# Optimization experiments

Hardware: AMD Instinct MI355X
Metric: run time of the kernel (lower is better)

Reference implementation:

```python
import jax, jax.numpy as jnp
import numpy as np

N_LAYERS = 3
FEATS = 128
POS = 3
M_DIM = 64
E_IN = 1 + 2 * FEATS          # 257 (rel_dist + x_i + x_j)
N_NODES = 20000
N_EDGES = 320000
LN_EPS = 1e-5


def _xavier(key, shape):
    fan_in, fan_out = shape[0], shape[1]
    std = (2.0 / (fan_in + fan_out)) ** 0.5
    return jax.random.normal(key, shape, dtype=jnp.float32) * std


def setup_inputs() -> dict:
    key = jax.random.key(0)
    ks = jax.random.split(key, 10)
    x = jax.random.normal(ks[0], (N_NODES, POS + FEATS), dtype=jnp.float32)
    edge_index = jax.random.randint(ks[1], (2, N_EDGES), 0, N_NODES)
    L = N_LAYERS
    def stack(k, shape):
        return jax.vmap(lambda kk: _xavier(kk, shape))(jax.random.split(k, L))
    params = {
        "ew1": stack(ks[2], (E_IN, 2 * E_IN)),      # edge_mlp linear 1
        "eb1": jnp.zeros((L, 2 * E_IN), jnp.float32),
        "ew2": stack(ks[3], (2 * E_IN, M_DIM)),      # edge_mlp linear 2
        "eb2": jnp.zeros((L, M_DIM), jnp.float32),
        "ng": jnp.ones((L, FEATS), jnp.float32),     # node LayerNorm gamma
        "nb": jnp.zeros((L, FEATS), jnp.float32),    # node LayerNorm beta
        "nw1": stack(ks[4], (FEATS + M_DIM, 2 * FEATS)),
        "nb1": jnp.zeros((L, 2 * FEATS), jnp.float32),
        "nw2": stack(ks[5], (2 * FEATS, FEATS)),
        "nb2": jnp.zeros((L, FEATS), jnp.float32),
        "cw1": stack(ks[6], (M_DIM, 4 * M_DIM)),
        "cb1": jnp.zeros((L, 4 * M_DIM), jnp.float32),
        "cw2": stack(ks[7], (4 * M_DIM, 1)),
        "cb2": jnp.zeros((L, 1), jnp.float32),
    }
    return {"x": x, "edge_index": edge_index, **params}


def _layer(x, edge_index, ew1, eb1, ew2, eb2, ng, nb, nw1, nb1, nw2, nb2,
           cw1, cb1, cw2, cb2):
    coors, feats = x[:, :POS], x[:, POS:]
    src, dst = edge_index[0], edge_index[1]
    # relative geometry per edge
    rel_coors = coors[src] - coors[dst]                       # [E, 3]
    rel_dist = jnp.sum(rel_coors * rel_coors, axis=-1, keepdims=True)  # [E, 1]
    # message MLP: cat[x_i (target), x_j (source), rel_dist]
    e_in = jnp.concatenate([feats[dst], feats[src], rel_dist], axis=-1)
    h = jax.nn.silu(e_in @ ew1 + eb1)
    m_ij = jax.nn.silu(h @ ew2 + eb2)                         # [E, m_dim]
    # coordinate update
    coor_w = jax.nn.silu(m_ij @ cw1 + cb1) @ cw2 + cb2        # [E, 1]
    mhat = jax.ops.segment_sum(coor_w * rel_coors, dst, num_segments=N_NODES)
    coors_out = coors + mhat
    # feature update (LayerNorm then MLP, residual)
    m_i = jax.ops.segment_sum(m_ij, dst, num_segments=N_NODES)
    mu = jnp.mean(feats, axis=-1, keepdims=True)
    var = jnp.mean((feats - mu) ** 2, axis=-1, keepdims=True)
    feats_n = (feats - mu) * jax.lax.rsqrt(var + LN_EPS) * ng + nb
    n_in = jnp.concatenate([feats_n, m_i], axis=-1)
    nh = jax.nn.silu(n_in @ nw1 + nb1) @ nw2 + nb2
    feats_out = feats + nh
    return jnp.concatenate([coors_out, feats_out], axis=-1)


def reference(x, edge_index, ew1, eb1, ew2, eb2, ng, nb, nw1, nb1, nw2, nb2,
              cw1, cb1, cw2, cb2):
    for l in range(N_LAYERS):
        x = _layer(x, edge_index,
                   ew1[l], eb1[l], ew2[l], eb2[l],
                   ng[l], nb[l], nw1[l], nb1[l], nw2[l], nb2[l],
                   cw1[l], cb1[l], cw2[l], cb2[l])
    return x
```

## Files before the change

### kernel.cpp

```cpp
#include <hip/hip_runtime.h>

typedef unsigned short u16;
typedef unsigned int   u32;
typedef __attribute__((ext_vector_type(2))) u32  u32x2;
typedef __attribute__((ext_vector_type(4))) u32  u32x4;
typedef __attribute__((ext_vector_type(8))) __bf16 bf16x8;
typedef __attribute__((ext_vector_type(4))) float  f32x4;

#define NN 20000
#define NE 320000
#define XD 131
#define F  128
#define MD 64
#define H1 514
#define H1P 544
#define NCH 17

#define GAS __attribute__((address_space(1)))
#define LAS __attribute__((address_space(3)))
#define LGKM0 asm volatile("s_waitcnt lgkmcnt(0)" ::: "memory")
#define VM0   asm volatile("s_waitcnt vmcnt(0)" ::: "memory")

__device__ __forceinline__ float silu(float a) {
    float e = __expf(-a);
    return a * __builtin_amdgcn_rcpf(1.0f + e);
}

__device__ __forceinline__ u16 f2bf(float f) {
    u32 u = __builtin_bit_cast(u32, f);
    return (u16)((u + 0x7FFFu + ((u >> 16) & 1u)) >> 16);
}
__device__ __forceinline__ u16 bfc(float f) { return __builtin_bit_cast(u16, (__bf16)f); }
__device__ __forceinline__ u32 pk2(float a, float b) {
    return (u32)bfc(a) | ((u32)bfc(b) << 16);
}
__device__ __forceinline__ bf16x8 mk8(u32 a, u32 b, u32 c, u32 d) {
    u32x4 t = {a, b, c, d};
    return __builtin_bit_cast(bf16x8, t);
}
__device__ __forceinline__ f32x4 mfma16(bf16x8 a, bf16x8 b, f32x4 c) {
    return __builtin_amdgcn_mfma_f32_16x16x32_bf16(a, b, c, 0, 0, 0);
}


__global__ void prep_w1(const float* __restrict__ ew1, const float* __restrict__ eb1,
                        u16* __restrict__ w1b, float* __restrict__ bias2) {
    int i = blockIdx.x * 256 + threadIdx.x;
    if (i >= 3 * H1P * 256) return;
    int k = i & 255;
    int n = (i >> 8) % H1P;
    int l = (i >> 8) / H1P;
    float v = (n < H1) ? ew1[(size_t)l * 257 * H1 + (size_t)k * H1 + n] : 0.f;
    w1b[(size_t)(l * H1P + n) * 256 + (k ^ ((n & 7) << 3))] = f2bf(v);
    if (k == 0) {
        bias2[(l * H1P + n) * 2 + 0] = (n < H1) ? eb1[l * H1 + n] : 0.f;
        bias2[(l * H1P + n) * 2 + 1] = (n < H1) ? ew1[(size_t)l * 257 * H1 + (size_t)256 * H1 + n] : 0.f;
    }
}

__global__ void prep_w2(const float* __restrict__ ew2, u16* __restrict__ w2b) {
    int i = blockIdx.x * 256 + threadIdx.x;
    if (i >= 3 * 64 * H1P) return;
    int k = i % H1P;
    int n = (i / H1P) & 63;
    int l = i / (H1P * 64);
    float v = (k < H1) ? ew2[(size_t)l * H1 * 64 + (size_t)k * 64 + n] : 0.f;
    w2b[(size_t)(l * 64 + n) * H1P + k] = f2bf(v);
}

__global__ void prep_cw1(const float* __restrict__ cw1, u16* __restrict__ cw1b) {
    int i = blockIdx.x * 256 + threadIdx.x;
    if (i >= 3 * 256 * 64) return;
    int k = i & 63;
    int n = (i >> 6) & 255;
    int l = i >> 14;
    cw1b[(size_t)l * 16384 + n * 64 + k] = f2bf(cw1[(size_t)l * 16384 + k * 256 + n]);
}

__global__ void prep_nw1(const float* __restrict__ nw1, u16* __restrict__ nw1b) {
    int i = blockIdx.x * 256 + threadIdx.x;
    if (i >= 3 * 256 * 192) return;
    int k = i % 192;
    int n = (i / 192) & 255;
    int l = i / (192 * 256);
    nw1b[(size_t)(l * 256 + n) * 192 + k] = f2bf(nw1[(size_t)l * 192 * 256 + (size_t)k * 256 + n]);
}

__global__ void prep_nw2(const float* __restrict__ nw2, u16* __restrict__ nw2b) {
    int i = blockIdx.x * 256 + threadIdx.x;
    if (i >= 3 * 128 * 256) return;
    int k = i & 255;
    int n = (i >> 8) & 127;
    int l = i >> 15;
    nw2b[(size_t)(l * 128 + n) * 256 + k] = f2bf(nw2[(size_t)l * 256 * 128 + (size_t)k * 128 + n]);
}

__global__ void x2bf(const float* __restrict__ xc, u32* __restrict__ xbf) {
    int i = blockIdx.x * 256 + threadIdx.x;
    if (i >= NN * 64) return;
    const int node = i >> 6, p = i & 63;
    const float a = xc[(size_t)node * XD + 3 + 2 * p];
    const float b = xc[(size_t)node * XD + 4 + 2 * p];
    xbf[(size_t)node * 64 + p] = pk2(a, b);
}


__global__ void csr_hist(const int* __restrict__ eidx, int* __restrict__ cnt) {
    int e = blockIdx.x * 256 + threadIdx.x;
    if (e < NE) atomicAdd(&cnt[eidx[NE + e]], 1);
}

__global__ void csr_scan(const int* __restrict__ cnt, int* __restrict__ rowp) {
    __shared__ int ps[1024];
    const int t = threadIdx.x;
    const int base = t * 20;
    int loc[20];
    int s = 0;
    #pragma unroll
    for (int i = 0; i < 20; ++i) {
        const int idx = base + i;
        const int c = (idx < NN) ? cnt[idx] : 0;
        loc[i] = s;
        s += c;
    }
    ps[t] = s;
    __syncthreads();
    for (int off = 1; off < 1024; off <<= 1) {
        int v = (t >= off) ? ps[t - off] : 0;
        __syncthreads();
        ps[t] += v;
        __syncthreads();
    }
    const int segbase = (t > 0) ? ps[t - 1] : 0;
    #pragma unroll
    for (int i = 0; i < 20; ++i) {
        const int idx = base + i;
        if (idx < NN) rowp[idx] = segbase + loc[i];
    }
    if (t == 1023) rowp[NN] = ps[1023];
}

__global__ void csr_fill(const int* __restrict__ eidx, const int* __restrict__ rowp,
                         int* __restrict__ fill, int* __restrict__ eids) {
    int e = blockIdx.x * 256 + threadIdx.x;
    if (e >= NE) return;
    const int d = eidx[NE + e];
    const int pos = atomicAdd(&fill[d], 1);
    eids[rowp[d] + pos] = e;
}


__global__ __launch_bounds__(256, 4) void reduce_mi(
    const u16* __restrict__ gmij, const int* __restrict__ rowp,
    const int* __restrict__ eids, float* __restrict__ m_i) {
    const int tid = threadIdx.x;
    const int n = blockIdx.x * 4 + (tid >> 6);
    const int c = tid & 63;
    if (n >= NN) return;
    const int b = rowp[n], e = rowp[n + 1];
    float acc = 0.f;
    for (int j = b; j < e; ++j) {
        const int eid = eids[j];
        const u16 v = gmij[(size_t)eid * 64 + c];
        acc += __builtin_bit_cast(float, (u32)v << 16);
    }
    m_i[(size_t)n * 64 + c] = acc;
}


__global__ __launch_bounds__(256, 3) void edge_mfma(
    const float* __restrict__ x, const u16* __restrict__ xbf, const int* __restrict__ eidx,
    const char* __restrict__ w1b, const float* __restrict__ bias2,
    const char* __restrict__ w2b, const float* __restrict__ eb2,
    const char* __restrict__ cw1b, const float* __restrict__ cb1,
    const float* __restrict__ cw2, const float* __restrict__ cb2,
    float* __restrict__ m_i, float* __restrict__ mhat, u16* __restrict__ gmij)
{
    __shared__ __align__(16) char LDS[45568];
    const int tid = threadIdx.x;
    const int w = tid >> 6, l = tid & 63, lg = l >> 4, lc = l & 15;
    const int ebase = blockIdx.x * 128 + w * 32;
    char*  HT  = LDS + 32768 + w * 2560;
    char*  MJ  = LDS + w * 4352;
    float* RDS = (float*)(LDS + 43008);
    int*   SDS = (int*)(LDS + 45056);
    char*  STG = LDS + w * 8192;

    if (l < 32) {
        const int e = ebase + l;
        const int s = eidx[e], d = eidx[NE + e];
        const float ax = x[(size_t)s * XD + 0] - x[(size_t)d * XD + 0];
        const float ay = x[(size_t)s * XD + 1] - x[(size_t)d * XD + 1];
        const float az = x[(size_t)s * XD + 2] - x[(size_t)d * XD + 2];
        f32x4 v = {ax, ay, az, ax * ax + ay * ay + az * az};
        *(f32x4*)(RDS + (w * 32 + l) * 4) = v;
        SDS[w * 32 + l] = d;
    }

    bf16x8 A[2][8];
    const int r4 = l >> 4;
    #pragma unroll
    for (int p = 0; p < 2; ++p) {
        const int ebs = (p ? 0 : NE) + ebase;
        #pragma unroll
        for (int j = 0; j < 8; ++j) {
            const int r = j * 4 + r4;
            const int node = eidx[ebs + r];
            const int cp = lc ^ (r & 7);
            __builtin_amdgcn_global_load_lds((const GAS u32*)(xbf + (size_t)node * 128 + cp * 8),
                                             (LAS u32*)(STG + j * 1024), 16, 0, 0);
        }
        VM0;
        #pragma unroll
        for (int kt = 0; kt < 4; ++kt)
            #pragma unroll
            for (int et = 0; et < 2; ++et) {
                const int R = et * 16 + lc;
                A[et][p * 4 + kt] = *(bf16x8*)(STG + R * 256 + ((kt * 64 + lg * 16) ^ ((R & 7) << 4)));
            }
        LGKM0;
    }

    float rd_e[2];
    rd_e[0] = RDS[(w * 32 + lc) * 4 + 3];
    rd_e[1] = RDS[(w * 32 + 16 + lc) * 4 + 3];
    LGKM0;

    __syncthreads();

    f32x4 c2[2][4];
    #pragma unroll
    for (int nt = 0; nt < 4; ++nt) {
        const float b = eb2[nt * 16 + lc];
        c2[0][nt] = (f32x4){b, b, b, b};
        c2[1][nt] = (f32x4){b, b, b, b};
    }

    {
        const char* g = w1b + (size_t)w * 4096;
        #pragma unroll
        for (int r = 0; r < 4; ++r)
            __builtin_amdgcn_global_load_lds((const GAS u32*)(g + r * 1024 + l * 16),
                                             (LAS u32*)(LDS + w * 4096 + r * 1024), 16, 0, 0);
    }

    const float* pB = bias2;
    #pragma unroll 1
    for (int ch = 0; ch < NCH; ++ch) {
        VM0;
        __syncthreads();
        if (ch + 1 < NCH) {
            const char* g = w1b + (size_t)(ch + 1) * 16384 + w * 4096;
            char* dst = LDS + ((ch + 1) & 1) * 16384 + w * 4096;
            #pragma unroll
            for (int r = 0; r < 4; ++r)
                __builtin_amdgcn_global_load_lds((const GAS u32*)(g + r * 1024 + l * 16),
                                                 (LAS u32*)(dst + r * 1024), 16, 0, 0);
        }
        char* Bc = LDS + (ch & 1) * 16384;

        #pragma unroll
        for (int nt = 0; nt < 2; ++nt) {
            const float* bp = pB + (nt * 16 + lg * 4) * 2;
            f32x4 q0 = *(const f32x4*)(bp);
            f32x4 q1 = *(const f32x4*)(bp + 4);
            f32x4 c10, c11;
            c10[0] = fmaf(rd_e[0], q0[1], q0[0]); c10[1] = fmaf(rd_e[0], q0[3], q0[2]);
            c10[2] = fmaf(rd_e[0], q1[1], q1[0]); c10[3] = fmaf(rd_e[0], q1[3], q1[2]);
            c11[0] = fmaf(rd_e[1], q0[1], q0[0]); c11[1] = fmaf(rd_e[1], q0[3], q0[2]);
            c11[2] = fmaf(rd_e[1], q1[1], q1[0]); c11[3] = fmaf(rd_e[1], q1[3], q1[2]);
            const int nl = nt * 16 + lc;
            #pragma unroll
            for (int kt = 0; kt < 8; ++kt) {
                bf16x8 Wf = *(bf16x8*)(Bc + nl * 512 + ((kt * 64 + lg * 16) ^ ((nl & 7) << 4)));
                c10 = mfma16(Wf, A[0][kt], c10);
                c11 = mfma16(Wf, A[1][kt], c11);
            }
            u32x2 v0, v1;
            v0[0] = pk2(silu(c10[0]), silu(c10[1])); v0[1] = pk2(silu(c10[2]), silu(c10[3]));
            v1[0] = pk2(silu(c11[0]), silu(c11[1])); v1[1] = pk2(silu(c11[2]), silu(c11[3]));
            *(u32x2*)(HT + lc * 80 + nt * 32 + lg * 8) = v0;
            *(u32x2*)(HT + (16 + lc) * 80 + nt * 32 + lg * 8) = v1;
        }
        LGKM0;
        bf16x8 A2[2];
        A2[0] = *(bf16x8*)(HT + lc * 80 + lg * 16);
        A2[1] = *(bf16x8*)(HT + (16 + lc) * 80 + lg * 16);
        #pragma unroll
        for (int nt = 0; nt < 4; ++nt) {
            bf16x8 Bw = __builtin_bit_cast(bf16x8,
                *(const u32x4*)(w2b + (size_t)(nt * 16 + lc) * 1088 + ch * 64 + lg * 16));
            c2[0][nt] = mfma16(A2[0], Bw, c2[0][nt]);
            c2[1][nt] = mfma16(A2[1], Bw, c2[1][nt]);
        }
        pB += 64;
    }

    __syncthreads();

    int dstn[2][4];
    #pragma unroll
    for (int mt = 0; mt < 2; ++mt)
        #pragma unroll
        for (int r = 0; r < 4; ++r)
            dstn[mt][r] = SDS[w * 32 + mt * 16 + lg * 4 + r];

    #pragma unroll
    for (int mt = 0; mt < 2; ++mt)
        #pragma unroll
        for (int nt = 0; nt < 4; ++nt)
            #pragma unroll
            for (int r = 0; r < 4; ++r) {
                const float v = silu(c2[mt][nt][r]);
                const int rowl = mt * 16 + lg * 4 + r;
                const int col  = nt * 16 + lc;
                *(u16*)(MJ + rowl * 136 + col * 2) = bfc(v);
                if (!gmij) atomicAdd(m_i + (size_t)dstn[mt][r] * 64 + col, v);
            }
    LGKM0;

    if (gmij) {
        u16* grow = gmij + (size_t)ebase * 64;
        #pragma unroll
        for (int i = 0; i < 4; ++i) {
            const int row = i * 8 + (l >> 3);
            u32x4 v = *(u32x4*)(MJ + row * 136 + (l & 7) * 16);
            *(u32x4*)(grow + (size_t)row * 64 + (l & 7) * 8) = v;
        }
    }

    bf16x8 A3[2][2];
    #pragma unroll
    for (int mt = 0; mt < 2; ++mt)
        #pragma unroll
        for (int kt = 0; kt < 2; ++kt)
            A3[mt][kt] = *(bf16x8*)(MJ + (mt * 16 + lc) * 136 + kt * 64 + lg * 16);

    float pw[2][4] = {{0.f, 0.f, 0.f, 0.f}, {0.f, 0.f, 0.f, 0.f}};
    #pragma unroll 4
    for (int ct3 = 0; ct3 < 16; ++ct3) {
        const int col = ct3 * 16 + lc;
        const float b = cb1[col];
        f32x4 c30 = {b, b, b, b}, c31 = {b, b, b, b};
        #pragma unroll
        for (int kt = 0; kt < 2; ++kt) {
            bf16x8 B = __builtin_bit_cast(bf16x8,
                *(const u32x4*)(cw1b + (size_t)col * 128 + kt * 64 + lg * 16));
            c30 = mfma16(A3[0][kt], B, c30);
            c31 = mfma16(A3[1][kt], B, c31);
        }
        const float w2v = cw2[col];
        #pragma unroll
        for (int r = 0; r < 4; ++r) {
            pw[0][r] = fmaf(silu(c30[r]), w2v, pw[0][r]);
            pw[1][r] = fmaf(silu(c31[r]), w2v, pw[1][r]);
        }
    }
    #pragma unroll
    for (int m = 1; m < 16; m <<= 1)
        #pragma unroll
        for (int mt = 0; mt < 2; ++mt)
            #pragma unroll
            for (int r = 0; r < 4; ++r)
                pw[mt][r] += __shfl_xor(pw[mt][r], m, 64);

    const float cb2v = cb2[0];
    if (lc < 3) {
        #pragma unroll
        for (int mt = 0; mt < 2; ++mt)
            #pragma unroll
            for (int r = 0; r < 4; ++r) {
                const int rowl = mt * 16 + lg * 4 + r;
                const float cwv = pw[mt][r] + cb2v;
                atomicAdd(mhat + (size_t)dstn[mt][r] * 3 + lc,
                          cwv * RDS[(w * 32 + rowl) * 4 + lc]);
            }
    }
}


__global__ __launch_bounds__(256, 2) void node_mfma(
    const float* __restrict__ xc, const float* __restrict__ m_i, const float* __restrict__ mh,
    const float* __restrict__ ng, const float* __restrict__ nb,
    const char* __restrict__ nw1b, const float* __restrict__ nb1,
    const char* __restrict__ nw2b, const float* __restrict__ nb2,
    float* __restrict__ xn)
{
    __shared__ __align__(16) char LDS[4 * 4352];
    const int tid = threadIdx.x;
    const int w = tid >> 6, l = tid & 63, lg = l >> 4, lc = l & 15;
    char* HB = LDS + w * 4352;
    const int nb0 = blockIdx.x * 128 + w * 32;

    int nodes[2]; bool valid[2];
    #pragma unroll
    for (int et = 0; et < 2; ++et) {
        int n = nb0 + et * 16 + lc;
        valid[et] = (n < NN);
        nodes[et] = valid[et] ? n : (NN - 1);
    }

    bf16x8 BF[2][6];
    #pragma unroll
    for (int et = 0; et < 2; ++et) {
        const float* xr = xc + (size_t)nodes[et] * XD + 3;
        float v[4][8];
        float s = 0.f, q = 0.f;
        #pragma unroll
        for (int kt = 0; kt < 4; ++kt) {
            const int k0 = kt * 32 + lg * 8;
            #pragma unroll
            for (int j = 0; j < 8; ++j) {
                const float t = xr[k0 + j];
                v[kt][j] = t; s += t; q = fmaf(t, t, q);
            }
        }
        s += __shfl_xor(s, 16, 64); s += __shfl_xor(s, 32, 64);
        q += __shfl_xor(q, 16, 64); q += __shfl_xor(q, 32, 64);
        const float mu = s * (1.f / 128.f);
        const float rs = rsqrtf(q * (1.f / 128.f) - mu * mu + 1e-5f);
        #pragma unroll
        for (int kt = 0; kt < 4; ++kt) {
            const int k0 = kt * 32 + lg * 8;
            float4 g0 = *(const float4*)(ng + k0), g1 = *(const float4*)(ng + k0 + 4);
            float4 b0 = *(const float4*)(nb + k0), b1 = *(const float4*)(nb + k0 + 4);
            const u32 u0 = pk2((v[kt][0] - mu) * rs * g0.x + b0.x, (v[kt][1] - mu) * rs * g0.y + b0.y);
            const u32 u1 = pk2((v[kt][2] - mu) * rs * g0.z + b0.z, (v[kt][3] - mu) * rs * g0.w + b0.w);
            const u32 u2 = pk2((v[kt][4] - mu) * rs * g1.x + b1.x, (v[kt][5] - mu) * rs * g1.y + b1.y);
            const u32 u3 = pk2((v[kt][6] - mu) * rs * g1.z + b1.z, (v[kt][7] - mu) * rs * g1.w + b1.w);
            BF[et][kt] = mk8(u0, u1, u2, u3);
        }
        const float* mr = m_i + (size_t)nodes[et] * 64;
        #pragma unroll
        for (int kt2 = 0; kt2 < 2; ++kt2) {
            float4 a = *(const float4*)(mr + kt2 * 32 + lg * 8);
            float4 b = *(const float4*)(mr + kt2 * 32 + lg * 8 + 4);
            BF[et][4 + kt2] = mk8(pk2(a.x, a.y), pk2(a.z, a.w), pk2(b.x, b.y), pk2(b.z, b.w));
        }
    }

    f32x4 a2[8][2];
    #pragma unroll
    for (int ct2 = 0; ct2 < 8; ++ct2) {
        f32x4 b = *(const f32x4*)(nb2 + ct2 * 16 + lg * 4);
        a2[ct2][0] = b; a2[ct2][1] = b;
    }

    #pragma unroll 1
    for (int g = 0; g < 4; ++g) {
        f32x4 a1[4][2];
        #pragma unroll
        for (int ct = 0; ct < 4; ++ct) {
            f32x4 b = *(const f32x4*)(nb1 + g * 64 + ct * 16 + lg * 4);
            a1[ct][0] = b; a1[ct][1] = b;
        }
        #pragma unroll
        for (int ct = 0; ct < 4; ++ct)
            #pragma unroll
            for (int kt = 0; kt < 6; ++kt) {
                bf16x8 Aw = __builtin_bit_cast(bf16x8, *(const u32x4*)(
                    nw1b + (size_t)(g * 64 + ct * 16 + lc) * 384 + kt * 64 + lg * 16));
                a1[ct][0] = mfma16(Aw, BF[0][kt], a1[ct][0]);
                a1[ct][1] = mfma16(Aw, BF[1][kt], a1[ct][1]);
            }
        #pragma unroll
        for (int ct = 0; ct < 4; ++ct)
            #pragma unroll
            for (int et = 0; et < 2; ++et) {
                f32x4 c = a1[ct][et];
                u32 v0 = pk2(silu(c[0]), silu(c[1]));
                u32 v1 = pk2(silu(c[2]), silu(c[3]));
                *(u32*)(HB + (et * 16 + lc) * 136 + ct * 32 + lg * 8) = v0;
                *(u32*)(HB + (et * 16 + lc) * 136 + ct * 32 + lg * 8 + 4) = v1;
            }
        LGKM0;
        __builtin_amdgcn_sched_barrier(0);
        bf16x8 B2[2][2];
        #pragma unroll
        for (int et = 0; et < 2; ++et)
            #pragma unroll
            for (int kt2 = 0; kt2 < 2; ++kt2) {
                u32 a = *(u32*)(HB + (et * 16 + lc) * 136 + kt2 * 64 + lg * 16);
                u32 b = *(u32*)(HB + (et * 16 + lc) * 136 + kt2 * 64 + lg * 16 + 4);
                u32 c = *(u32*)(HB + (et * 16 + lc) * 136 + kt2 * 64 + lg * 16 + 8);
                u32 d = *(u32*)(HB + (et * 16 + lc) * 136 + kt2 * 64 + lg * 16 + 12);
                B2[et][kt2] = mk8(a, b, c, d);
            }
        #pragma unroll
        for (int ct2 = 0; ct2 < 8; ++ct2)
            #pragma unroll
            for (int kt2 = 0; kt2 < 2; ++kt2) {
                bf16x8 Aw = __builtin_bit_cast(bf16x8, *(const u32x4*)(
                    nw2b + (size_t)(ct2 * 16 + lc) * 512 + (g * 64 + kt2 * 32 + lg * 8) * 2));
                a2[ct2][0] = mfma16(Aw, B2[0][kt2], a2[ct2][0]);
                a2[ct2][1] = mfma16(Aw, B2[1][kt2], a2[ct2][1]);
            }
        LGKM0;
        __builtin_amdgcn_sched_barrier(0);
    }

    #pragma unroll
    for (int et = 0; et < 2; ++et) {
        if (!valid[et]) continue;
        const size_t nr = (size_t)nodes[et] * XD;
        #pragma unroll
        for (int ct2 = 0; ct2 < 8; ++ct2)
            #pragma unroll
            for (int r = 0; r < 4; ++r) {
                const int col = ct2 * 16 + lg * 4 + r;
                xn[nr + 3 + col] = a2[ct2][et][r] + xc[nr + 3 + col];
            }
    }
    for (int idx = tid; idx < 384; idx += 256) {
        const int n = blockIdx.x * 128 + idx / 3;
        const int d = idx - (idx / 3) * 3;
        if (n < NN)
            xn[(size_t)n * XD + d] = xc[(size_t)n * XD + d] + mh[n * 3 + d];
    }
}


extern "C" void kernel_launch(void* const* d_in, const int* in_sizes, int n_in,
                              void* d_out, int out_size, void* d_ws, size_t ws_size,
                              hipStream_t stream) {
    const float* x_in = (const float*)d_in[0];
    const int*   eidx = (const int*)  d_in[1];
    const float* ew1  = (const float*)d_in[2];
    const float* eb1  = (const float*)d_in[3];
    const float* ew2  = (const float*)d_in[4];
    const float* eb2  = (const float*)d_in[5];
    const float* ng   = (const float*)d_in[6];
    const float* nb   = (const float*)d_in[7];
    const float* nw1  = (const float*)d_in[8];
    const float* nb1  = (const float*)d_in[9];
    const float* nw2  = (const float*)d_in[10];
    const float* nb2  = (const float*)d_in[11];
    const float* cw1  = (const float*)d_in[12];
    const float* cb1  = (const float*)d_in[13];
    const float* cw2  = (const float*)d_in[14];
    const float* cb2  = (const float*)d_in[15];
    float* out = (float*)d_out;

    char* ws = (char*)d_ws;
    size_t off = 0;
    auto alloc = [&](size_t bytes) { char* p = ws + off; off = (off + bytes + 255) & ~255ull; return p; };
    float* mi    = (float*)alloc((size_t)NN * MD * 4);
    float* mh    = (float*)alloc((size_t)NN * 3 * 4);
    u32*   xbf   = (u32*)  alloc((size_t)NN * 256);
    float* bias2 = (float*)alloc((size_t)3 * H1P * 8);
    char*  w1b   = alloc((size_t)3 * H1P * 512);
    char*  w2b   = alloc((size_t)3 * 64 * 1088);
    char*  cw1b  = alloc((size_t)3 * 256 * 128);
    char*  nw1b  = alloc((size_t)3 * 256 * 384);
    char*  nw2b  = alloc((size_t)3 * 128 * 512);
    u16* gmij = (u16*)alloc((size_t)NE * 64 * 2);
    int* rowp = (int*) alloc((size_t)(NN + 1) * 4);
    int* eids = (int*) alloc((size_t)NE * 4);
    int* cnt  = (int*) alloc((size_t)NN * 4);
    int* fillp= (int*) alloc((size_t)NN * 4);
    const bool two = (off <= ws_size);

    prep_w1 <<<(3 * H1P * 256 + 255) / 256, 256, 0, stream>>>(ew1, eb1, (u16*)w1b, bias2);
    prep_w2 <<<(3 * 64 * H1P + 255) / 256, 256, 0, stream>>>(ew2, (u16*)w2b);
    prep_cw1<<<(3 * 256 * 64 + 255) / 256, 256, 0, stream>>>(cw1, (u16*)cw1b);
    prep_nw1<<<(3 * 256 * 192 + 255) / 256, 256, 0, stream>>>(nw1, (u16*)nw1b);
    prep_nw2<<<(3 * 128 * 256 + 255) / 256, 256, 0, stream>>>(nw2, (u16*)nw2b);

    if (two) {
        hipMemsetAsync(cnt,  0, (size_t)NN * 4, stream);
        hipMemsetAsync(fillp,0, (size_t)NN * 4, stream);
        csr_hist<<<(NE + 255) / 256, 256, 0, stream>>>(eidx, cnt);
        csr_scan<<<1, 1024, 0, stream>>>(cnt, rowp);
        csr_fill<<<(NE + 255) / 256, 256, 0, stream>>>(eidx, rowp, fillp, eids);
    }

    for (int l = 0; l < 3; ++l) {
        const float* xc = (l == 0) ? x_in : out;
        float*       xn = out;
        if (!two) hipMemsetAsync(mi, 0, (size_t)NN * MD * 4, stream);
        hipMemsetAsync(mh, 0, (size_t)NN * 3 * 4, stream);
        x2bf<<<(NN * 64 + 255) / 256, 256, 0, stream>>>(xc, xbf);
        edge_mfma<<<NE / 128, 256, 0, stream>>>(
            xc, (const u16*)xbf, eidx,
            w1b + (size_t)l * H1P * 512, bias2 + (size_t)l * H1P * 2,
            w2b + (size_t)l * 64 * 1088, eb2 + (size_t)l * 64,
            cw1b + (size_t)l * 256 * 128, cb1 + (size_t)l * 256,
            cw2 + (size_t)l * 256, cb2 + l,
            mi, mh, two ? gmij : (u16*)nullptr);
        if (two)
            reduce_mi<<<(NN + 3) / 4, 256, 0, stream>>>(gmij, rowp, eids, mi);
        node_mfma<<<(NN + 127) / 128, 256, 0, stream>>>(
            xc, mi, mh,
            ng + (size_t)l * F, nb + (size_t)l * F,
            nw1b + (size_t)l * 256 * 384, nb1 + (size_t)l * 256,
            nw2b + (size_t)l * 128 * 512, nb2 + (size_t)l * F,
            xn);
    }
}
```

Baseline: 925.6 us.

## Process edges in destination-sorted order and reduce coordinate updates without atomics

Adds a one-time permutation of the edge list into CSR (destination-sorted) order so the edge kernel processes edges grouped by destination. Per-edge messages are then stored contiguously, and reduce_mi reads them sequentially instead of gathering through eids, using 32-bit paired loads. The coordinate update is written per edge to a buffer and summed in reduce_mi, which replaces the float atomicAdds and the per-layer memset. The cost is an extra per-edge buffer write and read, plus the sorted order changing the gather locality of source nodes.

```diff
diff --git a/kernel.cpp b/kernel.cpp
--- a/kernel.cpp
+++ b/kernel.cpp
@@ -149,32 +149,49 @@
     eids[rowp[d] + pos] = e;
 }
 
+__global__ void esort(const int* __restrict__ eidx, const int* __restrict__ eids,
+                      int* __restrict__ esrc, int* __restrict__ edst) {
+    int j = blockIdx.x * 256 + threadIdx.x;
+    if (j >= NE) return;
+    const int e = eids[j];
+    esrc[j] = eidx[e];
+    edst[j] = eidx[NE + e];
+}
+
 
 __global__ __launch_bounds__(256, 4) void reduce_mi(
-    const u16* __restrict__ gmij, const int* __restrict__ rowp,
-    const int* __restrict__ eids, float* __restrict__ m_i) {
+    const u16* __restrict__ gmij, const float* __restrict__ gmh,
+    const int* __restrict__ rowp, float* __restrict__ m_i, float* __restrict__ mh) {
     const int tid = threadIdx.x;
-    const int n = blockIdx.x * 4 + (tid >> 6);
-    const int c = tid & 63;
+    const int n = blockIdx.x * 8 + (tid >> 5);
+    const int t = tid & 31;
     if (n >= NN) return;
     const int b = rowp[n], e = rowp[n + 1];
-    float acc = 0.f;
+    float a0 = 0.f, a1 = 0.f;
     for (int j = b; j < e; ++j) {
-        const int eid = eids[j];
-        const u16 v = gmij[(size_t)eid * 64 + c];
-        acc += __builtin_bit_cast(float, (u32)v << 16);
-    }
-    m_i[(size_t)n * 64 + c] = acc;
+        const u32 v = *(const u32*)(gmij + (size_t)j * 64 + t * 2);
+        a0 += __builtin_bit_cast(float, v << 16);
+        a1 += __builtin_bit_cast(float, v & 0xFFFF0000u);
+    }
+    m_i[(size_t)n * 64 + 2 * t]     = a0;
+    m_i[(size_t)n * 64 + 2 * t + 1] = a1;
+    if (t < 3) {
+        float m = 0.f;
+        for (int j = b; j < e; ++j) m += gmh[(size_t)j * 4 + t];
+        mh[n * 3 + t] = m;
+    }
 }
 
 
 __global__ __launch_bounds__(256, 3) void edge_mfma(
-    const float* __restrict__ x, const u16* __restrict__ xbf, const int* __restrict__ eidx,
+    const float* __restrict__ x, const u16* __restrict__ xbf,
+    const int* __restrict__ esrc, const int* __restrict__ edst,
     const char* __restrict__ w1b, const float* __restrict__ bias2,
     const char* __restrict__ w2b, const float* __restrict__ eb2,
     const char* __restrict__ cw1b, const float* __restrict__ cb1,
     const float* __restrict__ cw2, const float* __restrict__ cb2,
-    float* __restrict__ m_i, float* __restrict__ mhat, u16* __restrict__ gmij)
+    float* __restrict__ m_i, float* __restrict__ mhat,
+    u16* __restrict__ gmij, float* __restrict__ gmh)
 {
     __shared__ __align__(16) char LDS[45568];
     const int tid = threadIdx.x;
@@ -188,7 +205,7 @@
 
     if (l < 32) {
         const int e = ebase + l;
-        const int s = eidx[e], d = eidx[NE + e];
+        const int s = esrc[e], d = edst[e];
         const float ax = x[(size_t)s * XD + 0] - x[(size_t)d * XD + 0];
         const float ay = x[(size_t)s * XD + 1] - x[(size_t)d * XD + 1];
         const float az = x[(size_t)s * XD + 2] - x[(size_t)d * XD + 2];
@@ -201,11 +218,11 @@
     const int r4 = l >> 4;
     #pragma unroll
     for (int p = 0; p < 2; ++p) {
-        const int ebs = (p ? 0 : NE) + ebase;
+        const int* ea = p ? esrc : edst;
         #pragma unroll
         for (int j = 0; j < 8; ++j) {
             const int r = j * 4 + r4;
-            const int node = eidx[ebs + r];
+            const int node = ea[ebase + r];
             const int cp = lc ^ (r & 7);
             __builtin_amdgcn_global_load_lds((const GAS u32*)(xbf + (size_t)node * 128 + cp * 8),
                                              (LAS u32*)(STG + j * 1024), 16, 0, 0);
@@ -372,8 +389,11 @@
             for (int r = 0; r < 4; ++r) {
                 const int rowl = mt * 16 + lg * 4 + r;
                 const float cwv = pw[mt][r] + cb2v;
-                atomicAdd(mhat + (size_t)dstn[mt][r] * 3 + lc,
-                          cwv * RDS[(w * 32 + rowl) * 4 + lc]);
+                const float contrib = cwv * RDS[(w * 32 + rowl) * 4 + lc];
+                if (gmij)
+                    gmh[(size_t)(ebase + rowl) * 4 + lc] = contrib;
+                else
+                    atomicAdd(mhat + (size_t)dstn[mt][r] * 3 + lc, contrib);
             }
     }
 }
@@ -554,8 +574,11 @@
     char*  nw1b  = alloc((size_t)3 * 256 * 384);
     char*  nw2b  = alloc((size_t)3 * 128 * 512);
     u16* gmij = (u16*)alloc((size_t)NE * 64 * 2);
+    float* gmh= (float*)alloc((size_t)NE * 4 * 4);
     int* rowp = (int*) alloc((size_t)(NN + 1) * 4);
     int* eids = (int*) alloc((size_t)NE * 4);
+    int* esrc = (int*) alloc((size_t)NE * 4);
+    int* edst = (int*) alloc((size_t)NE * 4);
     int* cnt  = (int*) alloc((size_t)NN * 4);
     int* fillp= (int*) alloc((size_t)NN * 4);
     const bool two = (off <= ws_size);
@@ -566,29 +589,35 @@
     prep_nw1<<<(3 * 256 * 192 + 255) / 256, 256, 0, stream>>>(nw1, (u16*)nw1b);
     prep_nw2<<<(3 * 128 * 256 + 255) / 256, 256, 0, stream>>>(nw2, (u16*)nw2b);
 
+    const int* esrcA = eidx;
+    const int* edstA = eidx + NE;
     if (two) {
         hipMemsetAsync(cnt,  0, (size_t)NN * 4, stream);
         hipMemsetAsync(fillp,0, (size_t)NN * 4, stream);
         csr_hist<<<(NE + 255) / 256, 256, 0, stream>>>(eidx, cnt);
         csr_scan<<<1, 1024, 0, stream>>>(cnt, rowp);
         csr_fill<<<(NE + 255) / 256, 256, 0, stream>>>(eidx, rowp, fillp, eids);
+        esort<<<(NE + 255) / 256, 256, 0, stream>>>(eidx, eids, esrc, edst);
+        esrcA = esrc; edstA = edst;
     }
 
     for (int l = 0; l < 3; ++l) {
         const float* xc = (l == 0) ? x_in : out;
         float*       xn = out;
-        if (!two) hipMemsetAsync(mi, 0, (size_t)NN * MD * 4, stream);
-        hipMemsetAsync(mh, 0, (size_t)NN * 3 * 4, stream);
+        if (!two) {
+            hipMemsetAsync(mi, 0, (size_t)NN * MD * 4, stream);
+            hipMemsetAsync(mh, 0, (size_t)NN * 3 * 4, stream);
+        }
         x2bf<<<(NN * 64 + 255) / 256, 256, 0, stream>>>(xc, xbf);
         edge_mfma<<<NE / 128, 256, 0, stream>>>(
-            xc, (const u16*)xbf, eidx,
+            xc, (const u16*)xbf, esrcA, edstA,
             w1b + (size_t)l * H1P * 512, bias2 + (size_t)l * H1P * 2,
             w2b + (size_t)l * 64 * 1088, eb2 + (size_t)l * 64,
             cw1b + (size_t)l * 256 * 128, cb1 + (size_t)l * 256,
             cw2 + (size_t)l * 256, cb2 + l,
-            mi, mh, two ? gmij : (u16*)nullptr);
+            mi, mh, two ? gmij : (u16*)nullptr, two ? gmh : (float*)nullptr);
         if (two)
-            reduce_mi<<<(NN + 3) / 4, 256, 0, stream>>>(gmij, rowp, eids, mi);
+            reduce_mi<<<(NN + 7) / 8, 256, 0, stream>>>(gmij, gmh, rowp, mi, mh);
         node_mfma<<<(NN + 127) / 128, 256, 0, stream>>>(
             xc, mi, mh,
             ng + (size_t)l * F, nb + (size_t)l * F,
```

Measured after the change: 857.8 us. 7.3% less time.
